# Kernel optimization log

Hardware: AMD Instinct MI355X
Metric: run time of the kernel (lower is better)

The kernel has to match this reference:

```python
import jax, jax.numpy as jnp
import numpy as np
import math

B, C, H, W = 8, 512, 32, 32
NH = 8           # num_heads
G = 32           # group norm groups
EPS = 1e-6


def group_norm(x, gamma, beta, groups=G, eps=EPS):
    # x: [B, C, H, W]
    b, c, h, w = x.shape
    xr = x.reshape(b, groups, c // groups, h, w)
    mu = xr.mean(axis=(2, 3, 4), keepdims=True)
    var = xr.var(axis=(2, 3, 4), keepdims=True)
    xn = ((xr - mu) * jax.lax.rsqrt(var + eps)).reshape(b, c, h, w)
    return xn * gamma[None, :, None, None] + beta[None, :, None, None]


def conv2d(x, w, b, pad):
    y = jax.lax.conv_general_dilated(
        x, w, window_strides=(1, 1), padding=[(pad, pad), (pad, pad)],
        dimension_numbers=("NCHW", "OIHW", "NCHW"))
    return y + b[None, :, None, None]


def setup_inputs() -> dict:
    key = jax.random.key(0)
    ks = jax.random.split(key, 20)
    def n(k, shape, s=0.02):
        return jax.random.normal(k, shape, dtype=jnp.float32) * s
    f32 = jnp.float32
    return {
        "hidden_states": jax.random.normal(ks[0], (B, C, H, W), dtype=f32),
        "pre_g": jnp.ones(C, f32), "pre_b": jnp.zeros(C, f32),
        "norm_g": jnp.ones(C, f32), "norm_b": jnp.zeros(C, f32),
        "post_g": jnp.ones(C, f32), "post_b": jnp.zeros(C, f32),
        "pos_emb": n(ks[1], (1, C, 32, 32)),
        "wq": n(ks[2], (C, C)), "wk": n(ks[3], (C, C)), "wv": n(ks[4], (C, C)),
        "wq0": n(ks[5], (C // 2, C)), "wq1": n(ks[6], (C // 2, C)),
        "wk0": n(ks[7], (C // 2, C)), "wk1": n(ks[8], (C // 2, C)),
        "wv0": n(ks[9], (C // 2, C)), "wv1": n(ks[10], (C // 2, C)),
        "sa_w1": n(ks[11], (C // 8, C, 1, 1)), "sa_b1": jnp.zeros(C // 8, f32),
        "sa_w2": n(ks[12], (C // 8, C // 8, 3, 3)), "sa_b2": jnp.zeros(C // 8, f32),
        "sa_w3": n(ks[13], (1, C // 8, 1, 1)), "sa_b3": jnp.zeros(1, f32),
        "ff_w1": n(ks[14], (C, 2 * C)), "ff_b1": jnp.zeros(C, f32),
        "ff_w2": n(ks[15], (C, C)), "ff_b2": jnp.zeros(C, f32),
        "out_w": n(ks[16], (C, C)), "out_b": jnp.zeros(C, f32),
    }


def reference(hidden_states, pre_g, pre_b, norm_g, norm_b, post_g, post_b,
              pos_emb, wq, wk, wv, wq0, wq1, wk0, wk1, wv0, wv1,
              sa_w1, sa_b1, sa_w2, sa_b2, sa_w3, sa_b3,
              ff_w1, ff_b1, ff_w2, ff_b2, out_w, out_b):
    b, c, h, w = hidden_states.shape
    S = h * w
    residual = hidden_states
    x = group_norm(hidden_states, pre_g, pre_b)
    # H == W == 32: bilinear interpolation of pos_emb to its own size is identity
    x = x + pos_emb
    # conv-based sigmoid spatial gate
    s1 = jax.nn.silu(conv2d(x, sa_w1, sa_b1, 0))
    s2 = jax.nn.silu(conv2d(s1, sa_w2, sa_b2, 1))
    spatial_weights = jax.nn.sigmoid(conv2d(s2, sa_w3, sa_b3, 0))  # [B,1,H,W]
    spatial_enhanced = x * spatial_weights
    # standard attention path (self-attention: encoder states = normed tokens)
    sh = group_norm(x, norm_g, norm_b).reshape(b, c, S).transpose(0, 2, 1)  # [B,S,C]
    enc = sh
    hd = c // NH
    def split_heads(t):
        return t.reshape(b, S, NH, hd).transpose(0, 2, 1, 3)  # [B,NH,S,hd]
    qh = split_heads(sh @ wq.T)
    kh = split_heads(enc @ wk.T)
    vh = split_heads(enc @ wv.T)
    scores = jnp.einsum("bhqd,bhkd->bhqk", qh, kh) / math.sqrt(hd)
    probs = jax.nn.softmax(scores, axis=-1)
    standard_out = jnp.einsum("bhqk,bhkd->bhqd", probs, vh)
    standard_out = standard_out.transpose(0, 2, 1, 3).reshape(b, S, c)
    # multi-scale attention paths over the spatially gated features (single head)
    msh = spatial_enhanced.reshape(b, c, S).transpose(0, 2, 1)  # [B,S,C]
    parts = []
    for wqm, wkm, wvm in ((wq0, wk0, wv0), (wq1, wk1, wv1)):
        qm = msh @ wqm.T      # [B,S,C/2]
        km = enc @ wkm.T
        vm = enc @ wvm.T
        sc = jnp.einsum("bqd,bkd->bqk", qm, km) / math.sqrt(qm.shape[-1])
        parts.append(jnp.einsum("bqk,bkd->bqd", jax.nn.softmax(sc, axis=-1), vm))
    multi_out = jnp.concatenate(parts, axis=-1)            # [B,S,C]
    combined = jnp.concatenate([standard_out, multi_out], axis=-1)  # [B,S,2C]
    fused = jax.nn.silu(combined @ ff_w1.T + ff_b1) @ ff_w2.T + ff_b2  # dropout = eval
    final = fused @ out_w.T + out_b
    final = final.transpose(0, 2, 1).reshape(b, c, h, w)
    final = group_norm(final, post_g, post_b)
    return final + residual
```

## Files before the change

### kernel.cpp

```cpp
#include <hip/hip_runtime.h>

typedef unsigned short u16;
typedef unsigned long long u64;
typedef __attribute__((ext_vector_type(8))) short s8v;
typedef __attribute__((ext_vector_type(4))) short s4v;
typedef __attribute__((ext_vector_type(4))) float f4v;

#define LOG2E 1.4426950408889634f

__device__ __forceinline__ float b2f(u16 u) {
  union { unsigned u; float f; } x; x.u = ((unsigned)u) << 16; return x.f;
}
__device__ __forceinline__ u16 f2b(float f) {
  union { float f; unsigned u; } x; x.f = f;
  unsigned r = x.u + 0x7fffu + ((x.u >> 16) & 1u);
  return (u16)(r >> 16);
}
__device__ __forceinline__ unsigned cvtpk(float lo, float hi) {
  unsigned r;
  asm("v_cvt_pk_bf16_f32 %0, %1, %2" : "=v"(r) : "v"(lo), "v"(hi));
  return r;
}

#define MFMA16(a, b, c) __builtin_amdgcn_mfma_f32_16x16x32_bf16((a), (b), (c), 0, 0, 0)

__device__ __forceinline__ void gload16(const void* g, void* l) {
  __builtin_amdgcn_global_load_lds(
      (const __attribute__((address_space(1))) unsigned*)g,
      (__attribute__((address_space(3))) unsigned*)l, 16, 0, 0);
}

struct Segs {
  const float* src[14];
  int cum[15];
  float scl[14];
};

__global__ __launch_bounds__(256) void castk(Segs sg, u16* __restrict__ dst) {
  int gid = (blockIdx.x * 256 + threadIdx.x) * 4;
  if (gid >= sg.cum[14]) return;
  int s = 0;
  while (gid >= sg.cum[s + 1]) ++s;
  const float* sp = sg.src[s] + (gid - sg.cum[s]);
  float sc = sg.scl[s];
  f4v v = *(const f4v*)sp;
  s4v o;
  o[0] = (short)f2b(v[0] * sc); o[1] = (short)f2b(v[1] * sc);
  o[2] = (short)f2b(v[2] * sc); o[3] = (short)f2b(v[3] * sc);
  *(s4v*)(dst + gid) = o;
}

__global__ __launch_bounds__(256) void gn1_k(
    const float* __restrict__ hs, const float* __restrict__ pg, const float* __restrict__ pb,
    const float* __restrict__ pos, u16* __restrict__ xb,
    float* __restrict__ mu2, float* __restrict__ rs2)
{
  int bid = blockIdx.x;
  int b = bid >> 5, g = bid & 31;
  int tid = threadIdx.x, l = tid & 63, w = tid >> 6;
  const float* src = hs + ((size_t)b * 512 + g * 16) * 1024;
  const float* pp = pos + (size_t)(g * 16) * 1024;
  u16* dst = xb + ((size_t)b * 512 + g * 16) * 1024;
  f4v vals[16];
  float sum = 0.f, sq = 0.f;
#pragma unroll
  for (int i = 0; i < 16; ++i) {
    int idx = tid + i * 256;
    vals[i] = *(const f4v*)(src + (size_t)idx * 4);
    f4v v = vals[i];
    sum += v[0] + v[1] + v[2] + v[3];
    sq += v[0] * v[0] + v[1] * v[1] + v[2] * v[2] + v[3] * v[3];
  }
  __shared__ float red[8];
#pragma unroll
  for (int off = 1; off < 64; off <<= 1) { sum += __shfl_xor(sum, off); sq += __shfl_xor(sq, off); }
  if (l == 0) { red[w * 2] = sum; red[w * 2 + 1] = sq; }
  __syncthreads();
  float S = red[0] + red[2] + red[4] + red[6];
  float Q = red[1] + red[3] + red[5] + red[7];
  float mean = S * (1.f / 16384.f);
  float var = Q * (1.f / 16384.f) - mean * mean;
  float rstd = rsqrtf(var + 1e-6f);
  __syncthreads();
  float sum2 = 0.f, sq2 = 0.f;
#pragma unroll
  for (int i = 0; i < 16; ++i) {
    int idx = tid + i * 256;
    int c = idx >> 8;
    float gam = pg[g * 16 + c], bet = pb[g * 16 + c];
    f4v v = vals[i];
    f4v pe = *(const f4v*)(pp + (size_t)idx * 4);
    f4v o;
    s4v ob;
#pragma unroll
    for (int j = 0; j < 4; ++j) {
      o[j] = (v[j] - mean) * rstd * gam + bet + pe[j];
      ob[j] = (short)f2b(o[j]);
    }
    *(s4v*)(dst + (size_t)idx * 4) = ob;
    sum2 += o[0] + o[1] + o[2] + o[3];
    sq2 += o[0] * o[0] + o[1] * o[1] + o[2] * o[2] + o[3] * o[3];
  }
#pragma unroll
  for (int off = 1; off < 64; off <<= 1) { sum2 += __shfl_xor(sum2, off); sq2 += __shfl_xor(sq2, off); }
  if (l == 0) { red[w * 2] = sum2; red[w * 2 + 1] = sq2; }
  __syncthreads();
  if (tid == 0) {
    float S2 = red[0] + red[2] + red[4] + red[6];
    float Q2 = red[1] + red[3] + red[5] + red[7];
    float m2 = S2 * (1.f / 16384.f);
    float v2 = Q2 * (1.f / 16384.f) - m2 * m2;
    mu2[b * 32 + g] = m2;
    rs2[b * 32 + g] = rsqrtf(v2 + 1e-6f);
  }
}

__global__ __launch_bounds__(256) void trans_gn2(
    const u16* __restrict__ xb, const float* __restrict__ mu2, const float* __restrict__ rs2,
    const float* __restrict__ ng, const float* __restrict__ nb,
    u16* __restrict__ xt, u16* __restrict__ sh)
{
  __shared__ float lds[512 * 17];
  int st = blockIdx.x, b = blockIdx.y;
  int tid = threadIdx.x;
  const u16* xp = xb + (size_t)b * 512 * 1024 + st * 16;
#pragma unroll
  for (int i = 0; i < 4; ++i) {
    int idx = tid + i * 256;
    int c = idx >> 1, sq = (idx & 1) * 8;
    s8v v = *(const s8v*)(xp + (size_t)c * 1024 + sq);
#pragma unroll
    for (int j = 0; j < 8; ++j) lds[c * 17 + sq + j] = b2f((u16)v[j]);
  }
  __syncthreads();
  int s = tid & 15, cb0 = (tid >> 4) * 32;
  size_t token = (size_t)b * 1024 + st * 16 + s;
  float m0 = mu2[b * 32 + (cb0 >> 4)], m1 = mu2[b * 32 + (cb0 >> 4) + 1];
  float r0 = rs2[b * 32 + (cb0 >> 4)], r1 = rs2[b * 32 + (cb0 >> 4) + 1];
#pragma unroll
  for (int q = 0; q < 4; ++q) {
    s8v ox, os;
#pragma unroll
    for (int j = 0; j < 8; ++j) {
      int cj = q * 8 + j;
      int c = cb0 + cj;
      float v = lds[c * 17 + s];
      ox[j] = (short)f2b(v);
      float mm = (cj < 16) ? m0 : m1;
      float rr = (cj < 16) ? r0 : r1;
      os[j] = (short)f2b((v - mm) * rr * ng[c] + nb[c]);
    }
    *(s8v*)(xt + token * 512 + cb0 + q * 8) = ox;
    *(s8v*)(sh + token * 512 + cb0 + q * 8) = os;
  }
}

template <int BM, int BN, bool SILU, bool OUT32, bool BIAS, bool RSCALE>
__global__ __launch_bounds__(256, 2) void gemm_k(
    const u16* __restrict__ A, int lda,
    const u16* __restrict__ Bw, int ldb,
    void* __restrict__ Cp, int ldc,
    const float* __restrict__ bias, int K, int ntx,
    const float* __restrict__ rscale)
{
  constexpr int WMT = BM / 2, WNT = BN / 2, MF = WMT / 16, NF = WNT / 16;
  __shared__ u16 Al[BM * 64];
  __shared__ u16 Bl[BN * 64];
  const int tid = threadIdx.x, l = tid & 63, w = tid >> 6;
  const int lg = l >> 4, lr = l & 15;
  const int wm = w >> 1, wn = w & 1;
  const int flat = blockIdx.x;
  const int cpx = gridDim.x >> 3;
  const int id = (flat & 7) * cpx + (flat >> 3);
  const int grp = id / (ntx * 4), rem = id % (ntx * 4);
  const int nt = rem >> 2, mt = grp * 4 + (rem & 3);
  const u16* Ag = A + (size_t)mt * BM * lda;
  const u16* Bg = Bw + (size_t)nt * BN * ldb;
  const f4v z = {0.f, 0.f, 0.f, 0.f};
  f4v acc[MF][NF];
#pragma unroll
  for (int i = 0; i < MF; ++i)
#pragma unroll
    for (int j = 0; j < NF; ++j) acc[i][j] = z;

  for (int kt = 0; kt < K; kt += 64) {
    __syncthreads();
    for (int f = tid; f < BM * 8; f += 256) {
      int row = f >> 3, g = (f & 7) ^ (row & 7);
      gload16(Ag + (size_t)row * lda + kt + g * 8, (char*)Al + f * 16);
    }
    for (int f = tid; f < BN * 8; f += 256) {
      int row = f >> 3, g = (f & 7) ^ (row & 7);
      gload16(Bg + (size_t)row * ldb + kt + g * 8, (char*)Bl + f * 16);
    }
    __syncthreads();
#pragma unroll
    for (int ks = 0; ks < 2; ++ks) {
      s8v af[MF], bf[NF];
#pragma unroll
      for (int mf = 0; mf < MF; ++mf) {
        int row = wm * WMT + mf * 16 + lr;
        af[mf] = *(const s8v*)((const char*)Al + row * 128 + (((ks * 4 + lg) ^ (row & 7)) << 4));
      }
#pragma unroll
      for (int nf = 0; nf < NF; ++nf) {
        int row = wn * WNT + nf * 16 + lr;
        bf[nf] = *(const s8v*)((const char*)Bl + row * 128 + (((ks * 4 + lg) ^ (row & 7)) << 4));
      }
#pragma unroll
      for (int mf = 0; mf < MF; ++mf)
#pragma unroll
        for (int nf = 0; nf < NF; ++nf)
          acc[mf][nf] = MFMA16(af[mf], bf[nf], acc[mf][nf]);
    }
  }
#pragma unroll
  for (int mf = 0; mf < MF; ++mf) {
    int row0 = mt * BM + wm * WMT + mf * 16 + lg * 4;
#pragma unroll
    for (int nf = 0; nf < NF; ++nf) {
      int col = nt * BN + wn * WNT + nf * 16 + lr;
      float bv = BIAS ? bias[col] : 0.f;
#pragma unroll
      for (int r = 0; r < 4; ++r) {
        float v = acc[mf][nf][r] + bv;
        if (RSCALE) v *= rscale[row0 + r];
        if (SILU) v = v / (1.f + exp2f(-v * LOG2E));
        size_t off = (size_t)(row0 + r) * ldc + col;
        if (OUT32) ((float*)Cp)[off] = v;
        else ((u16*)Cp)[off] = f2b(v);
      }
    }
  }
}

__global__ __launch_bounds__(256, 2) void gemm_gate_k(
    const u16* __restrict__ A, int lda,
    const u16* __restrict__ Bw, int ldb,
    const float* __restrict__ bias, int K,
    const float* __restrict__ w3, const float* __restrict__ b3,
    float* __restrict__ gate)
{
  constexpr int BM = 64, BN = 64, WMT = 32, WNT = 32, MF = 2, NF = 2;
  __shared__ u16 Al[BM * 64];
  __shared__ u16 Bl[BN * 64];
  __shared__ float gt[64][68];
  const int tid = threadIdx.x, l = tid & 63, w = tid >> 6;
  const int lg = l >> 4, lr = l & 15;
  const int wm = w >> 1, wn = w & 1;
  const int flat = blockIdx.x;
  const int cpx = gridDim.x >> 3;
  const int mt = (flat & 7) * cpx + (flat >> 3);
  const u16* Ag = A + (size_t)mt * BM * lda;
  const u16* Bg = Bw;
  const f4v z = {0.f, 0.f, 0.f, 0.f};
  f4v acc[MF][NF];
#pragma unroll
  for (int i = 0; i < MF; ++i)
#pragma unroll
    for (int j = 0; j < NF; ++j) acc[i][j] = z;

  for (int kt = 0; kt < K; kt += 64) {
    __syncthreads();
    for (int f = tid; f < BM * 8; f += 256) {
      int row = f >> 3, g = (f & 7) ^ (row & 7);
      gload16(Ag + (size_t)row * lda + kt + g * 8, (char*)Al + f * 16);
    }
    for (int f = tid; f < BN * 8; f += 256) {
      int row = f >> 3, g = (f & 7) ^ (row & 7);
      gload16(Bg + (size_t)row * ldb + kt + g * 8, (char*)Bl + f * 16);
    }
    __syncthreads();
#pragma unroll
    for (int ks = 0; ks < 2; ++ks) {
      s8v af[MF], bf[NF];
#pragma unroll
      for (int mf = 0; mf < MF; ++mf) {
        int row = wm * WMT + mf * 16 + lr;
        af[mf] = *(const s8v*)((const char*)Al + row * 128 + (((ks * 4 + lg) ^ (row & 7)) << 4));
      }
#pragma unroll
      for (int nf = 0; nf < NF; ++nf) {
        int row = wn * WNT + nf * 16 + lr;
        bf[nf] = *(const s8v*)((const char*)Bl + row * 128 + (((ks * 4 + lg) ^ (row & 7)) << 4));
      }
#pragma unroll
      for (int mf = 0; mf < MF; ++mf)
#pragma unroll
        for (int nf = 0; nf < NF; ++nf)
          acc[mf][nf] = MFMA16(af[mf], bf[nf], acc[mf][nf]);
    }
  }
  __syncthreads();
#pragma unroll
  for (int mf = 0; mf < MF; ++mf) {
    int lrow0 = wm * WMT + mf * 16 + lg * 4;
#pragma unroll
    for (int nf = 0; nf < NF; ++nf) {
      int col = wn * WNT + nf * 16 + lr;
      float bv = bias[col];
#pragma unroll
      for (int r = 0; r < 4; ++r) {
        float v = acc[mf][nf][r] + bv;
        v = v / (1.f + exp2f(-v * LOG2E));
        gt[lrow0 + r][col] = v;
      }
    }
  }
  __syncthreads();
  if (tid < 64) {
    float a = b3[0];
    for (int c = 0; c < 64; ++c) a += gt[tid][c] * w3[c];
    gate[mt * 64 + tid] = 1.f / (1.f + exp2f(-a * LOG2E));
  }
}

__global__ __launch_bounds__(256) void im2col_k(const u16* __restrict__ s1t, u16* __restrict__ col) {
  int gid = blockIdx.x * 256 + threadIdx.x;
  if (gid >= 8192 * 64) return;
  int token = gid >> 6, c = gid & 63;
  int s = token & 1023, y = s >> 5, xx = s & 31;
  u16* dst = col + (size_t)token * 576 + c * 9;
#pragma unroll
  for (int dy = 0; dy < 3; ++dy)
#pragma unroll
    for (int dx = 0; dx < 3; ++dx) {
      int yy = y + dy - 1, x2 = xx + dx - 1;
      u16 v = 0;
      if (yy >= 0 && yy < 32 && x2 >= 0 && x2 < 32)
        v = s1t[(size_t)(token + (dy - 1) * 32 + (dx - 1)) * 64 + c];
      dst[dy * 3 + dx] = v;
    }
}

__global__ __launch_bounds__(256) void tvm_k(const u16* __restrict__ proj,
                                             u16* __restrict__ vts, u16* __restrict__ vtm)
{
  __shared__ u16 tile[64][258];
  const int tid = threadIdx.x;
  const int kb = blockIdx.x, y = blockIdx.y;
  int hd, col0, b, hh;
  u16* outp;
  if (y < 64) { hd = 64; col0 = 1024; b = y >> 3; hh = y & 7; outp = vts + (size_t)y * 64 * 1024; }
  else { int y2 = y - 64; hd = 256; col0 = 2048; b = y2 >> 1; hh = y2 & 1; outp = vtm + (size_t)y2 * 256 * 1024; }
  const int hd8 = hd >> 3;
  const u16* src = proj + ((size_t)b * 1024 + kb * 64) * 2560 + col0 + hh * hd;
  for (int f = tid; f < 64 * hd8; f += 256) {
    int key = f / hd8, c = f % hd8;
    *(s8v*)&tile[key][c * 8] = *(const s8v*)(src + (size_t)key * 2560 + c * 8);
  }
  __syncthreads();
  u16* dst = outp + kb * 64;
  for (int idx = tid; idx < hd * 16; idx += 256) {
    int d = idx >> 4, a = idx & 15;
    u16 e0 = tile[a][d], e1 = tile[16 + a][d], e2 = tile[32 + a][d], e3 = tile[48 + a][d];
    u64 v = (u64)e0 | ((u64)e1 << 16) | ((u64)e2 << 32) | ((u64)e3 << 48);
    *(u64*)(dst + (size_t)d * 1024 + a * 4) = v;
  }
}

__global__ __launch_bounds__(256, 4) void attn_std(
    const u16* __restrict__ proj, const u16* __restrict__ vts, u16* __restrict__ comb)
{
  const int tid = threadIdx.x, l = tid & 63, w = tid >> 6;
  const int lg = l >> 4, lr = l & 15;
  const int flat = blockIdx.x;
  const int xcd = flat & 7, idx = flat >> 3;
  const int bh = xcd + 8 * (idx >> 4);
  const int qt = idx & 15;
  const int b = bh >> 3, h = bh & 7;
  const size_t tokb = (size_t)b * 1024;
  __shared__ u16 Kl[64 * 64];
  __shared__ u16 Vl[64 * 64];
  __shared__ u16 Pl[4][16 * 64];
  const int qr0 = qt * 64 + w * 16;
  s8v qf[2];
#pragma unroll
  for (int ks = 0; ks < 2; ++ks)
    qf[ks] = *(const s8v*)(proj + (tokb + qr0 + lr) * 2560 + h * 64 + ks * 32 + lg * 8);
  const f4v z = {0.f, 0.f, 0.f, 0.f};
  f4v acc[4];
  float lsl[4] = {0.f, 0.f, 0.f, 0.f};
#pragma unroll
  for (int r = 0; r < 4; ++r) acc[r] = z;

  const u16* gk[2];
  const u16* gv[2];
  char* lk[2];
  char* lv[2];
#pragma unroll
  for (int j = 0; j < 2; ++j) {
    int f = tid + j * 256;
    int key = f >> 3, g = (f & 7) ^ (key & 7);
    gk[j] = proj + (tokb + key) * 2560 + 512 + h * 64 + g * 8;
    int c = (f & 7) ^ (key & 7);
    gv[j] = vts + (size_t)bh * 64 * 1024 + (size_t)key * 1024 + c * 8;
    lk[j] = (char*)&Kl[0] + f * 16;
    lv[j] = (char*)&Vl[0] + f * 16;
  }

  for (int kt = 0; kt < 16; ++kt) {
    __syncthreads();
#pragma unroll
    for (int j = 0; j < 2; ++j) {
      gload16(gk[j], lk[j]);
      gload16(gv[j], lv[j]);
    }
#pragma unroll
    for (int j = 0; j < 2; ++j) { gk[j] += 64 * 2560; gv[j] += 64; }
    __syncthreads();
    f4v sf[4];
#pragma unroll
    for (int nf = 0; nf < 4; ++nf) sf[nf] = z;
    __builtin_amdgcn_s_setprio(1);
#pragma unroll
    for (int ks = 0; ks < 2; ++ks) {
      s8v kfr[4];
#pragma unroll
      for (int nf = 0; nf < 4; ++nf) {
        int row = nf * 16 + lr;
        kfr[nf] = *(const s8v*)((const char*)&Kl[0] + row * 128 + (((ks * 4 + lg) ^ (row & 7)) << 4));
      }
#pragma unroll
      for (int nf = 0; nf < 4; ++nf) sf[nf] = MFMA16(qf[ks], kfr[nf], sf[nf]);
    }
    __builtin_amdgcn_s_setprio(0);
#pragma unroll
    for (int r = 0; r < 4; ++r) {
      float pv[4];
#pragma unroll
      for (int nf = 0; nf < 4; ++nf) pv[nf] = exp2f(sf[nf][r]);
      lsl[r] += (pv[0] + pv[1]) + (pv[2] + pv[3]);
      int q = lg * 4 + r;
      u64 pk = (u64)cvtpk(pv[0], pv[1]) | ((u64)cvtpk(pv[2], pv[3]) << 32);
      *(u64*)((char*)&Pl[w][0] + q * 128 + ((((lr >> 1) ^ (q & 7)) << 4)) + (lr & 1) * 8) = pk;
    }
    __builtin_amdgcn_s_setprio(1);
#pragma unroll
    for (int ks2 = 0; ks2 < 2; ++ks2) {
      int g = ks2 * 4 + lg;
      s8v pfr = *(const s8v*)((const char*)&Pl[w][0] + lr * 128 + ((g ^ (lr & 7)) << 4));
#pragma unroll
      for (int nf = 0; nf < 4; ++nf) {
        int d = nf * 16 + lr;
        s8v vfr = *(const s8v*)((const char*)&Vl[0] + d * 128 + ((g ^ (d & 7)) << 4));
        acc[nf] = MFMA16(pfr, vfr, acc[nf]);
      }
    }
    __builtin_amdgcn_s_setprio(0);
  }
#pragma unroll
  for (int r = 0; r < 4; ++r) {
    float t = lsl[r];
#pragma unroll
    for (int off = 1; off < 16; off <<= 1) t += __shfl_xor(t, off);
    float inv = 1.f / t;
    size_t row = tokb + qr0 + lg * 4 + r;
#pragma unroll
    for (int nf = 0; nf < 4; ++nf)
      comb[row * 1024 + h * 64 + nf * 16 + lr] = f2b(acc[nf][r] * inv);
  }
}

__global__ __launch_bounds__(256, 2) void attn_ms(
    const u16* __restrict__ proj, const u16* __restrict__ qm, const u16* __restrict__ vtm,
    u16* __restrict__ pacc, float* __restrict__ pl)
{
  const int tid = threadIdx.x, l = tid & 63, w = tid >> 6;
  const int lg = l >> 4, lr = l & 15;
  const int flat = blockIdx.x;
  const int xcd = flat & 7, idx = flat >> 3;
  const int bp = xcd + 8 * (idx >> 5);
  const int rest = idx & 31;
  const int qt = rest >> 1, ks = rest & 1;
  const int b = bp >> 1, p = bp & 1;
  const size_t tokb = (size_t)b * 1024;
  __shared__ u16 Kl[64 * 256];
  __shared__ u16 Vl[256 * 64];
  __shared__ u16 Pl[4][16 * 64];
  const int qr0 = qt * 64 + w * 16;
  s8v qf[8];
#pragma unroll
  for (int kf = 0; kf < 8; ++kf)
    qf[kf] = *(const s8v*)(qm + (tokb + qr0 + lr) * 512 + p * 256 + kf * 32 + lg * 8);
  const f4v z = {0.f, 0.f, 0.f, 0.f};
  f4v acc[16];
#pragma unroll
  for (int i = 0; i < 16; ++i) acc[i] = z;
  float lsl[4] = {0.f, 0.f, 0.f, 0.f};
  const u16* vbase = vtm + (size_t)bp * 256 * 1024;

  const u16* gk[8];
  const u16* gv[8];
#pragma unroll
  for (int j = 0; j < 8; ++j) {
    int f = tid + j * 256;
    int key = f >> 5, pgc = f & 31;
    int g = (pgc & 24) | ((pgc & 7) ^ (key & 7));
    gk[j] = proj + (tokb + ks * 512 + key) * 2560 + 1536 + p * 256 + g * 8;
    int d = f >> 3, c = (f & 7) ^ (d & 7);
    gv[j] = vbase + (size_t)d * 1024 + ks * 512 + c * 8;
  }

  for (int kk = 0; kk < 8; ++kk) {
    __syncthreads();
#pragma unroll
    for (int j = 0; j < 8; ++j) gload16(gk[j], (char*)Kl + (tid + j * 256) * 16);
#pragma unroll
    for (int j = 0; j < 8; ++j) gload16(gv[j], (char*)Vl + (tid + j * 256) * 16);
#pragma unroll
    for (int j = 0; j < 8; ++j) { gk[j] += 64 * 2560; gv[j] += 64; }
    __syncthreads();
    f4v sf[4];
#pragma unroll
    for (int nf = 0; nf < 4; ++nf) sf[nf] = z;
    __builtin_amdgcn_s_setprio(1);
#pragma unroll
    for (int ksi = 0; ksi < 8; ++ksi) {
      s8v kfr[4];
#pragma unroll
      for (int nf = 0; nf < 4; ++nf) {
        int row = nf * 16 + lr;
        int g = ksi * 4 + lg;
        int pg2 = (g & 24) | ((g & 7) ^ (row & 7));
        kfr[nf] = *(const s8v*)((const char*)Kl + row * 512 + (pg2 << 4));
      }
#pragma unroll
      for (int nf = 0; nf < 4; ++nf) sf[nf] = MFMA16(qf[ksi], kfr[nf], sf[nf]);
    }
    __builtin_amdgcn_s_setprio(0);
#pragma unroll
    for (int r = 0; r < 4; ++r) {
      float pv[4];
#pragma unroll
      for (int nf = 0; nf < 4; ++nf) pv[nf] = exp2f(sf[nf][r]);
      lsl[r] += (pv[0] + pv[1]) + (pv[2] + pv[3]);
      int q = lg * 4 + r;
      u64 pk = (u64)cvtpk(pv[0], pv[1]) | ((u64)cvtpk(pv[2], pv[3]) << 32);
      *(u64*)((char*)&Pl[w][0] + q * 128 + ((((lr >> 1) ^ (q & 7)) << 4)) + (lr & 1) * 8) = pk;
    }
    __builtin_amdgcn_s_setprio(1);
#pragma unroll
    for (int ks2 = 0; ks2 < 2; ++ks2) {
      int g = ks2 * 4 + lg;
      s8v pfr = *(const s8v*)((const char*)&Pl[w][0] + lr * 128 + ((g ^ (lr & 7)) << 4));
#pragma unroll
      for (int nfd = 0; nfd < 16; ++nfd) {
        int d = nfd * 16 + lr;
        s8v vfr = *(const s8v*)((const char*)Vl + d * 128 + ((g ^ (d & 7)) << 4));
        acc[nfd] = MFMA16(pfr, vfr, acc[nfd]);
      }
    }
    __builtin_amdgcn_s_setprio(0);
  }
#pragma unroll
  for (int r = 0; r < 4; ++r) {
    float t = lsl[r];
#pragma unroll
    for (int off = 1; off < 16; off <<= 1) t += __shfl_xor(t, off);
    size_t prow = ((size_t)(bp * 2 + ks) * 16 + qt) * 64 + w * 16 + lg * 4 + r;
#pragma unroll
    for (int nfd = 0; nfd < 16; ++nfd)
      pacc[prow * 256 + nfd * 16 + lr] = f2b(acc[nfd][r]);
    if (lr == 0) pl[prow] = t;
  }
}

__global__ __launch_bounds__(256) void ms_comb(
    const u16* __restrict__ pacc, const float* __restrict__ pl,
    u16* __restrict__ comb)
{
  const int qt = blockIdx.x, bp = blockIdx.y;
  const int tid = threadIdx.x;
  const int row = tid >> 2, seg = tid & 3;
  size_t prow0 = ((size_t)(bp * 2 + 0) * 16 + qt) * 64 + row;
  size_t prow1 = ((size_t)(bp * 2 + 1) * 16 + qt) * 64 + row;
  float inv = 1.f / (pl[prow0] + pl[prow1]);
  const int b = bp >> 1, p = bp & 1;
  size_t orow = ((size_t)b * 1024 + qt * 64 + row) * 1024 + 512 + p * 256 + seg * 64;
#pragma unroll
  for (int j = 0; j < 8; ++j) {
    s8v v0 = *(const s8v*)(pacc + prow0 * 256 + seg * 64 + j * 8);
    s8v v1 = *(const s8v*)(pacc + prow1 * 256 + seg * 64 + j * 8);
    s8v ov;
#pragma unroll
    for (int e = 0; e < 8; ++e)
      ov[e] = (short)f2b((b2f((u16)v0[e]) + b2f((u16)v1[e])) * inv);
    *(s8v*)(comb + orow + j * 8) = ov;
  }
}

__global__ __launch_bounds__(256) void gn3_stats(
    const u16* __restrict__ fin, float* __restrict__ mu3, float* __restrict__ rs3)
{
  int bid = blockIdx.x;
  int b = bid >> 5, g = bid & 31;
  int tid = threadIdx.x, l = tid & 63, w = tid >> 6;
  const u16* fp = fin + (size_t)b * 1024 * 512 + g * 16;
  float sum = 0.f, sq = 0.f;
#pragma unroll
  for (int i = 0; i < 8; ++i) {
    int idx = tid + i * 256;
    int s = idx >> 1, half = (idx & 1) * 8;
    s8v v = *(const s8v*)(fp + (size_t)s * 512 + half);
#pragma unroll
    for (int e = 0; e < 8; ++e) { float f = b2f((u16)v[e]); sum += f; sq += f * f; }
  }
  __shared__ float red[8];
#pragma unroll
  for (int off = 1; off < 64; off <<= 1) { sum += __shfl_xor(sum, off); sq += __shfl_xor(sq, off); }
  if (l == 0) { red[w * 2] = sum; red[w * 2 + 1] = sq; }
  __syncthreads();
  if (tid == 0) {
    float S = red[0] + red[2] + red[4] + red[6];
    float Q = red[1] + red[3] + red[5] + red[7];
    float mean = S * (1.f / 16384.f);
    float var = Q * (1.f / 16384.f) - mean * mean;
    mu3[b * 32 + g] = mean;
    rs3[b * 32 + g] = rsqrtf(var + 1e-6f);
  }
}

__global__ __launch_bounds__(256) void final_k(
    const u16* __restrict__ fin, const float* __restrict__ mu3, const float* __restrict__ rs3,
    const float* __restrict__ postg, const float* __restrict__ postb,
    const float* __restrict__ res, float* __restrict__ out)
{
  __shared__ float lds[16 * 513];
  int st = blockIdx.x, b = blockIdx.y;
  int tid = threadIdx.x;
  const u16* fp = fin + ((size_t)b * 1024 + st * 16) * 512;
#pragma unroll
  for (int i = 0; i < 4; ++i) {
    int idx = tid + i * 256;
    int s = idx >> 6, c8 = (idx & 63) * 8;
    s8v v = *(const s8v*)(fp + (size_t)s * 512 + c8);
#pragma unroll
    for (int j = 0; j < 8; ++j) lds[s * 513 + c8 + j] = b2f((u16)v[j]);
  }
  __syncthreads();
#pragma unroll
  for (int cc = 0; cc < 2; ++cc) {
    int c = tid * 2 + cc;
    int g = c >> 4;
    float m = mu3[b * 32 + g], rv = rs3[b * 32 + g];
    float ga = postg[c], be = postb[c];
    const float* rp = res + ((size_t)b * 512 + c) * 1024 + st * 16;
    float* op = out + ((size_t)b * 512 + c) * 1024 + st * 16;
#pragma unroll
    for (int q = 0; q < 4; ++q) {
      f4v rr = *(const f4v*)(rp + q * 4);
      f4v o;
#pragma unroll
      for (int j = 0; j < 4; ++j) {
        float v = lds[(q * 4 + j) * 513 + c];
        o[j] = (v - m) * rv * ga + be + rr[j];
      }
      *(f4v*)(op + q * 4) = o;
    }
  }
}

extern "C" void kernel_launch(void* const* d_in, const int* in_sizes, int n_in,
                              void* d_out, int out_size, void* d_ws, size_t ws_size,
                              hipStream_t stream) {
  (void)in_sizes; (void)n_in; (void)out_size; (void)ws_size;
  const float* hs     = (const float*)d_in[0];
  const float* pre_g  = (const float*)d_in[1];
  const float* pre_b  = (const float*)d_in[2];
  const float* norm_g = (const float*)d_in[3];
  const float* norm_b = (const float*)d_in[4];
  const float* post_g = (const float*)d_in[5];
  const float* post_b = (const float*)d_in[6];
  const float* pos    = (const float*)d_in[7];
  const float* sa_b1  = (const float*)d_in[18];
  const float* sa_b2  = (const float*)d_in[20];
  const float* sa_w3  = (const float*)d_in[21];
  const float* sa_b3  = (const float*)d_in[22];
  const float* ff_b1  = (const float*)d_in[24];
  const float* ff_b2  = (const float*)d_in[26];
  const float* out_b  = (const float*)d_in[28];

  char* ws = (char*)d_ws;
  size_t off = 0;
  auto alloc = [&](size_t bytes) -> void* {
    void* pp = ws + off;
    off += (bytes + 255) & ~(size_t)255;
    return pp;
  };
  float* x    = (float*)alloc((size_t)16777216);
  u16* sh     = (u16*)alloc((size_t)8388608);
  u16* xt     = (u16*)alloc((size_t)8388608);
  float* mu2  = (float*)alloc(1024);
  float* rs2  = (float*)alloc(1024);
  float* mu3  = (float*)alloc(1024);
  float* rs3  = (float*)alloc(1024);
  float* pl   = (float*)alloc(262144);
  u16* wcat   = (u16*)alloc((size_t)2691072 * 2);
  u16* proj   = (u16*)alloc((size_t)8192 * 2560 * 2);
  u16* qmb    = (u16*)alloc((size_t)8388608);
  u16* s1t    = (u16*)alloc((size_t)1048576);
  u16* colb   = (u16*)alloc((size_t)8192 * 576 * 2);
  float* gate = (float*)alloc((size_t)32768);
  u16* vtm    = (u16*)alloc((size_t)8388608);
  u16* comb   = (u16*)alloc((size_t)16777216);
  u16* f1     = (u16*)alloc((size_t)8388608);
  u16* f2     = (u16*)alloc((size_t)8388608);
  u16* xb     = (u16*)x;
  u16* pacc   = (u16*)x;
  u16* fin    = (u16*)x;
  u16* vts    = colb;

  u16* Wbig = wcat;
  u16* Wq01 = wcat + 1310720;
  u16* W1   = wcat + 1572864;
  u16* W2   = wcat + 1605632;
  u16* Wff1 = wcat + 1642496;
  u16* Wff2 = wcat + 2166784;
  u16* Wout = wcat + 2428928;

  Segs sg;
  const int srcidx[14] = {8, 9, 10, 13, 14, 15, 16, 11, 12, 17, 19, 23, 25, 27};
  const int segsz[14] = {262144, 262144, 262144, 131072, 131072, 131072, 131072,
                         131072, 131072, 32768, 36864, 524288, 262144, 262144};
  int cum = 0;
  for (int i = 0; i < 14; ++i) {
    sg.src[i] = (const float*)d_in[srcidx[i]];
    sg.cum[i] = cum;
    sg.scl[i] = 1.f;
    cum += segsz[i];
  }
  sg.cum[14] = cum;
  sg.scl[0] = 0.125f * LOG2E;
  sg.scl[7] = 0.0625f * LOG2E;
  sg.scl[8] = 0.0625f * LOG2E;

  dim3 blk(256);
  castk<<<2628, blk, 0, stream>>>(sg, wcat);
  gn1_k<<<256, blk, 0, stream>>>(hs, pre_g, pre_b, pos, xb, mu2, rs2);
  trans_gn2<<<dim3(64, 8), blk, 0, stream>>>(xb, mu2, rs2, norm_g, norm_b, xt, sh);
  gemm_k<128, 128, false, false, false, false><<<1280, blk, 0, stream>>>(
      sh, 512, Wbig, 512, proj, 2560, nullptr, 512, 20, nullptr);
  gemm_k<64, 64, true, false, true, false><<<128, blk, 0, stream>>>(
      xt, 512, W1, 512, s1t, 64, sa_b1, 512, 1, nullptr);
  im2col_k<<<2048, blk, 0, stream>>>(s1t, colb);
  gemm_gate_k<<<128, blk, 0, stream>>>(colb, 576, W2, 576, sa_b2, 576, sa_w3, sa_b3, gate);
  gemm_k<128, 64, false, false, false, true><<<512, blk, 0, stream>>>(
      xt, 512, Wq01, 512, qmb, 512, nullptr, 512, 8, gate);
  tvm_k<<<dim3(16, 80), blk, 0, stream>>>(proj, vts, vtm);
  attn_std<<<1024, blk, 0, stream>>>(proj, vts, comb);
  attn_ms<<<512, blk, 0, stream>>>(proj, qmb, vtm, pacc, pl);
  ms_comb<<<dim3(16, 16), blk, 0, stream>>>(pacc, pl, comb);
  gemm_k<128, 64, true, false, true, false><<<512, blk, 0, stream>>>(
      comb, 1024, Wff1, 1024, f1, 512, ff_b1, 1024, 8, nullptr);
  gemm_k<128, 64, false, false, true, false><<<512, blk, 0, stream>>>(
      f1, 512, Wff2, 512, f2, 512, ff_b2, 512, 8, nullptr);
  gemm_k<128, 64, false, false, true, false><<<512, blk, 0, stream>>>(
      f2, 512, Wout, 512, fin, 512, out_b, 512, 8, nullptr);
  gn3_stats<<<256, blk, 0, stream>>>(fin, mu3, rs3);
  final_k<<<dim3(64, 8), blk, 0, stream>>>(fin, mu3, rs3, post_g, post_b, hs, (float*)d_out);
}
```

Measured before the change: 244.2 us.

## Split multi-scale attention keys four ways and halve LDS tiles for occupancy

The multi-scale attention kernel now splits the key range into four chunks instead of two, doubling the grid to 1024 blocks. Each block stages K and V in two half-width passes, with extra barriers between them, which halves shared memory per block so four blocks can fit per CU. The combine kernel now sums four partial accumulators and normalizers. The aim is more parallelism and occupancy, at the cost of more partial-result traffic, extra synchronisation, and register pressure under the tighter launch bound. It also assumes the partial buffers were sized for four splits.

After: 311.0 us. 1.27x slower.

```diff
diff --git a/kernel.cpp b/kernel.cpp
--- a/kernel.cpp
+++ b/kernel.cpp
@@ -462,7 +462,7 @@
   }
 }
 
-__global__ __launch_bounds__(256, 2) void attn_ms(
+__global__ __launch_bounds__(256, 4) void attn_ms(
     const u16* __restrict__ proj, const u16* __restrict__ qm, const u16* __restrict__ vtm,
     u16* __restrict__ pacc, float* __restrict__ pl)
 {
@@ -470,13 +470,13 @@
   const int lg = l >> 4, lr = l & 15;
   const int flat = blockIdx.x;
   const int xcd = flat & 7, idx = flat >> 3;
-  const int bp = xcd + 8 * (idx >> 5);
-  const int rest = idx & 31;
-  const int qt = rest >> 1, ks = rest & 1;
+  const int bp = xcd + 8 * (idx >> 6);
+  const int rest = idx & 63;
+  const int qt = rest >> 2, ks = rest & 3;
   const int b = bp >> 1, p = bp & 1;
   const size_t tokb = (size_t)b * 1024;
-  __shared__ u16 Kl[64 * 256];
-  __shared__ u16 Vl[256 * 64];
+  __shared__ u16 Kl[64 * 128];
+  __shared__ u16 Vl[128 * 64];
   __shared__ u16 Pl[4][16 * 64];
   const int qr0 = qt * 64 + w * 16;
   s8v qf[8];
@@ -490,43 +490,60 @@
   float lsl[4] = {0.f, 0.f, 0.f, 0.f};
   const u16* vbase = vtm + (size_t)bp * 256 * 1024;
 
-  const u16* gk[8];
-  const u16* gv[8];
-#pragma unroll
-  for (int j = 0; j < 8; ++j) {
+  const u16* gkb[4];
+  const u16* gvb[4];
+#pragma unroll
+  for (int j = 0; j < 4; ++j) {
     int f = tid + j * 256;
-    int key = f >> 5, pgc = f & 31;
-    int g = (pgc & 24) | ((pgc & 7) ^ (key & 7));
-    gk[j] = proj + (tokb + ks * 512 + key) * 2560 + 1536 + p * 256 + g * 8;
+    int key = f >> 4, gc = f & 15;
+    int gsrc = (gc & 8) | ((gc & 7) ^ (key & 7));
+    gkb[j] = proj + (tokb + ks * 256 + key) * 2560 + 1536 + p * 256 + gsrc * 8;
     int d = f >> 3, c = (f & 7) ^ (d & 7);
-    gv[j] = vbase + (size_t)d * 1024 + ks * 512 + c * 8;
-  }
-
-  for (int kk = 0; kk < 8; ++kk) {
-    __syncthreads();
-#pragma unroll
-    for (int j = 0; j < 8; ++j) gload16(gk[j], (char*)Kl + (tid + j * 256) * 16);
-#pragma unroll
-    for (int j = 0; j < 8; ++j) gload16(gv[j], (char*)Vl + (tid + j * 256) * 16);
-#pragma unroll
-    for (int j = 0; j < 8; ++j) { gk[j] += 64 * 2560; gv[j] += 64; }
+    gvb[j] = vbase + (size_t)d * 1024 + ks * 256 + c * 8;
+  }
+
+  for (int kk = 0; kk < 4; ++kk) {
+    __syncthreads();
+#pragma unroll
+    for (int j = 0; j < 4; ++j) gload16(gkb[j], (char*)Kl + (tid + j * 256) * 16);
+#pragma unroll
+    for (int j = 0; j < 4; ++j) gload16(gvb[j], (char*)Vl + (tid + j * 256) * 16);
     __syncthreads();
     f4v sf[4];
 #pragma unroll
     for (int nf = 0; nf < 4; ++nf) sf[nf] = z;
     __builtin_amdgcn_s_setprio(1);
 #pragma unroll
-    for (int ksi = 0; ksi < 8; ++ksi) {
+    for (int ki = 0; ki < 4; ++ki) {
       s8v kfr[4];
 #pragma unroll
       for (int nf = 0; nf < 4; ++nf) {
         int row = nf * 16 + lr;
-        int g = ksi * 4 + lg;
-        int pg2 = (g & 24) | ((g & 7) ^ (row & 7));
-        kfr[nf] = *(const s8v*)((const char*)Kl + row * 512 + (pg2 << 4));
-      }
-#pragma unroll
-      for (int nf = 0; nf < 4; ++nf) sf[nf] = MFMA16(qf[ksi], kfr[nf], sf[nf]);
+        int g = ki * 4 + lg;
+        int pos = (g & 8) | ((g & 7) ^ (row & 7));
+        kfr[nf] = *(const s8v*)((const char*)Kl + row * 256 + (pos << 4));
+      }
+#pragma unroll
+      for (int nf = 0; nf < 4; ++nf) sf[nf] = MFMA16(qf[ki], kfr[nf], sf[nf]);
+    }
+    __builtin_amdgcn_s_setprio(0);
+    __syncthreads();
+#pragma unroll
+    for (int j = 0; j < 4; ++j) gload16(gkb[j] + 128, (char*)Kl + (tid + j * 256) * 16);
+    __syncthreads();
+    __builtin_amdgcn_s_setprio(1);
+#pragma unroll
+    for (int ki = 0; ki < 4; ++ki) {
+      s8v kfr[4];
+#pragma unroll
+      for (int nf = 0; nf < 4; ++nf) {
+        int row = nf * 16 + lr;
+        int g = ki * 4 + lg;
+        int pos = (g & 8) | ((g & 7) ^ (row & 7));
+        kfr[nf] = *(const s8v*)((const char*)Kl + row * 256 + (pos << 4));
+      }
+#pragma unroll
+      for (int nf = 0; nf < 4; ++nf) sf[nf] = MFMA16(qf[4 + ki], kfr[nf], sf[nf]);
     }
     __builtin_amdgcn_s_setprio(0);
 #pragma unroll
@@ -545,20 +562,39 @@
       int g = ks2 * 4 + lg;
       s8v pfr = *(const s8v*)((const char*)&Pl[w][0] + lr * 128 + ((g ^ (lr & 7)) << 4));
 #pragma unroll
-      for (int nfd = 0; nfd < 16; ++nfd) {
-        int d = nfd * 16 + lr;
+      for (int nfl = 0; nfl < 8; ++nfl) {
+        int d = nfl * 16 + lr;
         s8v vfr = *(const s8v*)((const char*)Vl + d * 128 + ((g ^ (d & 7)) << 4));
-        acc[nfd] = MFMA16(pfr, vfr, acc[nfd]);
+        acc[nfl] = MFMA16(pfr, vfr, acc[nfl]);
       }
     }
     __builtin_amdgcn_s_setprio(0);
+    __syncthreads();
+#pragma unroll
+    for (int j = 0; j < 4; ++j) gload16(gvb[j] + (size_t)128 * 1024, (char*)Vl + (tid + j * 256) * 16);
+    __syncthreads();
+    __builtin_amdgcn_s_setprio(1);
+#pragma unroll
+    for (int ks2 = 0; ks2 < 2; ++ks2) {
+      int g = ks2 * 4 + lg;
+      s8v pfr = *(const s8v*)((const char*)&Pl[w][0] + lr * 128 + ((g ^ (lr & 7)) << 4));
+#pragma unroll
+      for (int nfl = 0; nfl < 8; ++nfl) {
+        int d = nfl * 16 + lr;
+        s8v vfr = *(const s8v*)((const char*)Vl + d * 128 + ((g ^ (d & 7)) << 4));
+        acc[8 + nfl] = MFMA16(pfr, vfr, acc[8 + nfl]);
+      }
+    }
+    __builtin_amdgcn_s_setprio(0);
+#pragma unroll
+    for (int j = 0; j < 4; ++j) { gkb[j] += 64 * 2560; gvb[j] += 64; }
   }
 #pragma unroll
   for (int r = 0; r < 4; ++r) {
     float t = lsl[r];
 #pragma unroll
     for (int off = 1; off < 16; off <<= 1) t += __shfl_xor(t, off);
-    size_t prow = ((size_t)(bp * 2 + ks) * 16 + qt) * 64 + w * 16 + lg * 4 + r;
+    size_t prow = ((size_t)(bp * 4 + ks) * 16 + qt) * 64 + w * 16 + lg * 4 + r;
 #pragma unroll
     for (int nfd = 0; nfd < 16; ++nfd)
       pacc[prow * 256 + nfd * 16 + lr] = f2b(acc[nfd][r]);
@@ -573,19 +609,28 @@
   const int qt = blockIdx.x, bp = blockIdx.y;
   const int tid = threadIdx.x;
   const int row = tid >> 2, seg = tid & 3;
-  size_t prow0 = ((size_t)(bp * 2 + 0) * 16 + qt) * 64 + row;
-  size_t prow1 = ((size_t)(bp * 2 + 1) * 16 + qt) * 64 + row;
-  float inv = 1.f / (pl[prow0] + pl[prow1]);
+  size_t pr[4];
+  float L = 0.f;
+#pragma unroll
+  for (int s = 0; s < 4; ++s) {
+    pr[s] = ((size_t)(bp * 4 + s) * 16 + qt) * 64 + row;
+    L += pl[pr[s]];
+  }
+  float inv = 1.f / L;
   const int b = bp >> 1, p = bp & 1;
   size_t orow = ((size_t)b * 1024 + qt * 64 + row) * 1024 + 512 + p * 256 + seg * 64;
 #pragma unroll
   for (int j = 0; j < 8; ++j) {
-    s8v v0 = *(const s8v*)(pacc + prow0 * 256 + seg * 64 + j * 8);
-    s8v v1 = *(const s8v*)(pacc + prow1 * 256 + seg * 64 + j * 8);
+    float o[8] = {0.f, 0.f, 0.f, 0.f, 0.f, 0.f, 0.f, 0.f};
+#pragma unroll
+    for (int s = 0; s < 4; ++s) {
+      s8v v = *(const s8v*)(pacc + pr[s] * 256 + seg * 64 + j * 8);
+#pragma unroll
+      for (int e = 0; e < 8; ++e) o[e] += b2f((u16)v[e]);
+    }
     s8v ov;
 #pragma unroll
-    for (int e = 0; e < 8; ++e)
-      ov[e] = (short)f2b((b2f((u16)v0[e]) + b2f((u16)v1[e])) * inv);
+    for (int e = 0; e < 8; ++e) ov[e] = (short)f2b(o[e] * inv);
     *(s8v*)(comb + orow + j * 8) = ov;
   }
 }
@@ -749,7 +794,7 @@
       xt, 512, Wq01, 512, qmb, 512, nullptr, 512, 8, gate);
   tvm_k<<<dim3(16, 80), blk, 0, stream>>>(proj, vts, vtm);
   attn_std<<<1024, blk, 0, stream>>>(proj, vts, comb);
-  attn_ms<<<512, blk, 0, stream>>>(proj, qmb, vtm, pacc, pl);
+  attn_ms<<<1024, blk, 0, stream>>>(proj, qmb, vtm, pacc, pl);
   ms_comb<<<dim3(16, 16), blk, 0, stream>>>(pacc, pl, comb);
   gemm_k<128, 64, true, false, true, false><<<512, blk, 0, stream>>>(
       comb, 1024, Wff1, 1024, f1, 512, ff_b1, 1024, 8, nullptr);
```
